# Kernel optimization log

Measured on AMD Instinct MI355X. Metric: run time of the kernel, lower is better.

## Reference

```python
import jax, jax.numpy as jnp
import numpy as np

DIM = 1024
HEADS = 16
DIM_HEAD = DIM // HEADS

def setup_inputs() -> dict:
    key = jax.random.key(0)
    k1, k2, k3 = jax.random.split(key, 3)
    x = jax.random.normal(k1, (2, 2048, DIM), dtype=jnp.float32)
    # nn.Linear(dim, 3*dim, bias=False): weight [3*dim, dim]; y = x @ W.T
    W_qkv = jax.random.normal(k2, (3 * DIM, DIM), dtype=jnp.float32) * (1.0 / np.sqrt(DIM))
    W_out = jax.random.normal(k3, (DIM, DIM), dtype=jnp.float32) * (1.0 / np.sqrt(DIM))
    return {"x": x, "W_qkv": W_qkv, "W_out": W_out}

def reference(x, W_qkv, W_out):
    b, s, _ = x.shape
    scale = DIM_HEAD ** -0.5
    qkv = x @ W_qkv.T                              # [b, s, 3*dim]
    q, k, v = jnp.split(qkv, 3, axis=-1)
    def to_heads(t):
        return t.reshape(b, s, HEADS, DIM_HEAD).transpose(0, 2, 1, 3)  # [b,h,s,d]
    q, k, v = map(to_heads, (q, k, v))
    scores = jnp.einsum('bhid,bhjd->bhij', q, k) * scale
    causal_mask = jnp.triu(jnp.ones((s, s), dtype=bool), k=1)
    scores = jnp.where(causal_mask, -jnp.inf, scores)
    attn = jax.nn.softmax(scores, axis=-1)
    out = jnp.einsum('bhij,bhjd->bhid', attn, v)
    out = out.transpose(0, 2, 1, 3).reshape(b, s, HEADS * DIM_HEAD)
    return out @ W_out.T
```

## Files before the change

### kernel.cpp

```cpp
#include <hip/hip_runtime.h>
#include <hip/hip_bf16.h>
#include <math.h>

using bf16 = __hip_bfloat16;
typedef __attribute__((ext_vector_type(8))) short bf16x8;
typedef __attribute__((ext_vector_type(4))) short bf16x4;
typedef __attribute__((ext_vector_type(4))) float f32x4;
typedef __attribute__((ext_vector_type(2))) int i32x2;

static __device__ __forceinline__ void gl_lds16(const void* g, void* l) {
  __builtin_amdgcn_global_load_lds(
      (const __attribute__((address_space(1))) unsigned int*)g,
      (__attribute__((address_space(3))) unsigned int*)l, 16, 0, 0);
}

#define MFMA16 __builtin_amdgcn_mfma_f32_16x16x32_bf16
#define MFMA16K16 __builtin_amdgcn_mfma_f32_16x16x16bf16_1k

static __device__ __forceinline__ short f2bf(float f) {
  return (short)((__builtin_bit_cast(unsigned int, f) + 0x8000u) >> 16);
}

__global__ __launch_bounds__(256) void cvt_all(
    const float* __restrict__ x, const float* __restrict__ wqkv,
    const float* __restrict__ wout, bf16* __restrict__ xb,
    bf16* __restrict__ wqkvb, bf16* __restrict__ woutb) {
  const int blk = blockIdx.x;
  const float* src;
  bf16* dst;
  int base;
  if (blk < 4096) {
    src = x; dst = xb; base = blk;
  } else if (blk < 7168) {
    src = wqkv; dst = wqkvb; base = blk - 4096;
  } else {
    src = wout; dst = woutb; base = blk - 7168;
  }
  const int i = (base * 256 + threadIdx.x) * 4;
  const float4 v = *(const float4*)(src + i);
  bf16x4 o;
  o.x = f2bf(v.x);
  o.y = f2bf(v.y);
  o.z = f2bf(v.z);
  o.w = f2bf(v.w);
  *(bf16x4*)(dst + i) = o;
}

template <int K>
static __device__ __forceinline__ void gemm_bt_acc(
    const bf16* __restrict__ A, const bf16* __restrict__ B,
    int rowA0, int rowB0, bf16* As, bf16* Bs, f32x4 acc[4][4]) {
  const int t = threadIdx.x;
  const int w = t >> 6, l = t & 63;
  const int quad = l >> 4, l16 = l & 15;
  const int wm = (w >> 1) * 64, wn = (w & 1) * 64;
  const int c0 = t, c1 = t + 256;
  const bf16* a0 = A + (size_t)(rowA0 + (c0 >> 2)) * K + (c0 & 3) * 8;
  const bf16* a1 = A + (size_t)(rowA0 + (c1 >> 2)) * K + (c1 & 3) * 8;
  const bf16* b0 = B + (size_t)(rowB0 + (c0 >> 2)) * K + (c0 & 3) * 8;
  const bf16* b1 = B + (size_t)(rowB0 + (c1 >> 2)) * K + (c1 & 3) * 8;
  for (int k0 = 0; k0 < K; k0 += 32) {
    __syncthreads();
    gl_lds16(a0 + k0, As + c0 * 8);
    gl_lds16(a1 + k0, As + c1 * 8);
    gl_lds16(b0 + k0, Bs + c0 * 8);
    gl_lds16(b1 + k0, Bs + c1 * 8);
    __syncthreads();
    bf16x8 af[4], bg[4];
#pragma unroll
    for (int i = 0; i < 4; i++)
      af[i] = *(const bf16x8*)(As + (wm + i * 16 + l16) * 32 + quad * 8);
#pragma unroll
    for (int j = 0; j < 4; j++)
      bg[j] = *(const bf16x8*)(Bs + (wn + j * 16 + l16) * 32 + quad * 8);
#pragma unroll
    for (int i = 0; i < 4; i++)
#pragma unroll
      for (int j = 0; j < 4; j++)
        acc[i][j] = MFMA16(af[i], bg[j], acc[i][j], 0, 0, 0);
  }
}

__global__ __launch_bounds__(256) void qkv_gemm(
    const bf16* __restrict__ x, const bf16* __restrict__ Wqkv,
    bf16* __restrict__ Qb, bf16* __restrict__ Kb, bf16* __restrict__ Vt) {
  __shared__ bf16 As[128 * 32];
  __shared__ bf16 Bs[128 * 32];
  f32x4 acc[4][4];
#pragma unroll
  for (int i = 0; i < 4; i++)
#pragma unroll
    for (int j = 0; j < 4; j++) acc[i][j] = (f32x4){0.f, 0.f, 0.f, 0.f};
  const int bm = blockIdx.x, bn = blockIdx.y;
  gemm_bt_acc<1024>(x, Wqkv, bm * 128, bn * 128, As, Bs, acc);

  const int t = threadIdx.x, w = t >> 6, l = t & 63;
  const int quad = l >> 4, l16 = l & 15;
  const int wm = (w >> 1) * 64, wn = (w & 1) * 64;
#pragma unroll
  for (int i = 0; i < 4; i++) {
#pragma unroll
    for (int j = 0; j < 4; j++) {
      const int n = bn * 128 + wn + j * 16 + l16;
      const int which = n >> 10;
      const int nn = n & 1023;
      const int h = nn >> 6, d = nn & 63;
      const float sc = (which == 0) ? 0.125f : 1.0f;
#pragma unroll
      for (int r = 0; r < 4; r++) {
        const int m = bm * 128 + wm + i * 16 + quad * 4 + r;
        const int b = m >> 11, s = m & 2047;
        const int bh = b * 16 + h;
        const bf16 v = __float2bfloat16(acc[i][j][r] * sc);
        if (which == 0)
          Qb[((size_t)bh * 2048 + s) * 64 + d] = v;
        else if (which == 1)
          Kb[((size_t)bh * 2048 + s) * 64 + d] = v;
        else
          Vt[((size_t)bh * 64 + d) * 2048 + s] = v;
      }
    }
  }
}

__global__ __launch_bounds__(256) void attn_kernel(
    const bf16* __restrict__ Qb, const bf16* __restrict__ Kb,
    const bf16* __restrict__ Vt, bf16* __restrict__ attn) {
  __shared__ bf16 Qs[64 * 64];
  __shared__ bf16 Ks[128 * 64];
  __shared__ bf16 Vts[64 * 128];
  const int x = blockIdx.x;
  const int bh = x & 31;
  const int idx = x >> 5;
  const int qt = (idx < 16) ? idx : 47 - idx;
  const int q0 = qt * 64;
  const int t = threadIdx.x, w = t >> 6, l = t & 63;
  const int quad = l >> 4, l16 = l & 15;
  const bf16x4 ones = {16256, 16256, 16256, 16256};

  const bf16* Qg = Qb + ((size_t)bh * 2048 + q0) * 64;
#pragma unroll
  for (int c = t; c < 512; c += 256) {
    const int row = c >> 3, pos = c & 7;
    gl_lds16(Qg + (row * 8 + (pos ^ (row & 7))) * 8, Qs + c * 8);
  }

  f32x4 oacc[4];
  f32x4 lacc = (f32x4){0.f, 0.f, 0.f, 0.f};
#pragma unroll
  for (int md = 0; md < 4; md++) oacc[md] = (f32x4){0.f, 0.f, 0.f, 0.f};

  const int njj = (qt + 2) >> 1;
  for (int jj = 0; jj < njj; jj++) {
    const int j0 = jj * 128;
    __syncthreads();
    const bf16* Kg = Kb + ((size_t)bh * 2048 + j0) * 64;
#pragma unroll
    for (int c = t; c < 1024; c += 256) {
      const int row = c >> 3, pos = c & 7;
      gl_lds16(Kg + (row * 8 + (pos ^ (row & 7))) * 8, Ks + c * 8);
    }
    const bf16* Vg = Vt + (size_t)bh * 64 * 2048 + j0;
#pragma unroll
    for (int c = t; c < 1024; c += 256) {
      const int d = c >> 4, pos = c & 15;
      gl_lds16(Vg + (size_t)d * 2048 + ((pos ^ (d & 15)) * 8), Vts + c * 8);
    }
    __syncthreads();

    f32x4 sacc[8];
#pragma unroll
    for (int mt = 0; mt < 8; mt++) sacc[mt] = (f32x4){0.f, 0.f, 0.f, 0.f};
#pragma unroll
    for (int kk = 0; kk < 2; kk++) {
      const int qrow = w * 16 + l16;
      const int qpos = (kk * 4 + quad) ^ (qrow & 7);
      bf16x8 qf = *(const bf16x8*)(Qs + qrow * 64 + qpos * 8);
#pragma unroll
      for (int mt = 0; mt < 8; mt++) {
        const int row = mt * 16 + l16;
        const int pos = (kk * 4 + quad) ^ (row & 7);
        bf16x8 kf = *(const bf16x8*)(Ks + row * 64 + pos * 8);
        sacc[mt] = MFMA16(kf, qf, sacc[mt], 0, 0, 0);
      }
    }

    bf16x4 pfrag[8];
    if (jj == njj - 1) {
      const int qi = q0 + w * 16 + l16;
#pragma unroll
      for (int mt = 0; mt < 8; mt++) {
        unsigned rb[4];
#pragma unroll
        for (int r = 0; r < 4; r++) {
          const int sg = j0 + mt * 16 + quad * 4 + r;
          const float p = (sg <= qi) ? __expf(sacc[mt][r]) : 0.f;
          rb[r] = __builtin_bit_cast(unsigned, p) + 0x8000u;
        }
        i32x2 pk;
        pk.x = (int)__builtin_amdgcn_perm(rb[1], rb[0], 0x07060302u);
        pk.y = (int)__builtin_amdgcn_perm(rb[3], rb[2], 0x07060302u);
        pfrag[mt] = __builtin_bit_cast(bf16x4, pk);
      }
    } else {
#pragma unroll
      for (int mt = 0; mt < 8; mt++) {
        unsigned rb[4];
#pragma unroll
        for (int r = 0; r < 4; r++) {
          const float p = __expf(sacc[mt][r]);
          rb[r] = __builtin_bit_cast(unsigned, p) + 0x8000u;
        }
        i32x2 pk;
        pk.x = (int)__builtin_amdgcn_perm(rb[1], rb[0], 0x07060302u);
        pk.y = (int)__builtin_amdgcn_perm(rb[3], rb[2], 0x07060302u);
        pfrag[mt] = __builtin_bit_cast(bf16x4, pk);
      }
    }

#pragma unroll
    for (int kt = 0; kt < 8; kt++) {
      lacc = MFMA16K16(ones, pfrag[kt], lacc, 0, 0, 0);
#pragma unroll
      for (int md = 0; md < 4; md++) {
        const int d = md * 16 + l16;
        const int pos = (kt * 2 + (quad >> 1)) ^ (d & 15);
        bf16x4 va = *(const bf16x4*)(Vts + d * 128 + pos * 8 + (quad & 1) * 4);
        oacc[md] = MFMA16K16(va, pfrag[kt], oacc[md], 0, 0, 0);
      }
    }
  }

  const float inv = 1.0f / lacc[0];
  const int b = bh >> 4, h = bh & 15;
  const int srow = q0 + w * 16 + l16;
#pragma unroll
  for (int md = 0; md < 4; md++) {
    bf16x4 o4;
#pragma unroll
    for (int r = 0; r < 4; r++) o4[r] = f2bf(oacc[md][r] * inv);
    *(bf16x4*)(attn + ((size_t)b * 2048 + srow) * 1024 + h * 64 + md * 16 +
               quad * 4) = o4;
  }
}

__global__ __launch_bounds__(256) void out_gemm(
    const bf16* __restrict__ attn, const bf16* __restrict__ Wout,
    float* __restrict__ out) {
  __shared__ bf16 As[128 * 32];
  __shared__ bf16 Bs[64 * 32];
  f32x4 acc[4][2];
#pragma unroll
  for (int i = 0; i < 4; i++)
#pragma unroll
    for (int j = 0; j < 2; j++) acc[i][j] = (f32x4){0.f, 0.f, 0.f, 0.f};
  const int bm = blockIdx.x, bn = blockIdx.y;
  const int t = threadIdx.x, w = t >> 6, l = t & 63;
  const int quad = l >> 4, l16 = l & 15;
  const int wm = (w >> 1) * 64, wn = (w & 1) * 32;
  const int c0 = t, c1 = t + 256;
  const bf16* a0 = attn + (size_t)(bm * 128 + (c0 >> 2)) * 1024 + (c0 & 3) * 8;
  const bf16* a1 = attn + (size_t)(bm * 128 + (c1 >> 2)) * 1024 + (c1 & 3) * 8;
  const bf16* b0 = Wout + (size_t)(bn * 64 + (t >> 2)) * 1024 + (t & 3) * 8;
  for (int k0 = 0; k0 < 1024; k0 += 32) {
    __syncthreads();
    gl_lds16(a0 + k0, As + c0 * 8);
    gl_lds16(a1 + k0, As + c1 * 8);
    gl_lds16(b0 + k0, Bs + t * 8);
    __syncthreads();
    bf16x8 af[4], bg[2];
#pragma unroll
    for (int i = 0; i < 4; i++)
      af[i] = *(const bf16x8*)(As + (wm + i * 16 + l16) * 32 + quad * 8);
#pragma unroll
    for (int j = 0; j < 2; j++)
      bg[j] = *(const bf16x8*)(Bs + (wn + j * 16 + l16) * 32 + quad * 8);
#pragma unroll
    for (int i = 0; i < 4; i++)
#pragma unroll
      for (int j = 0; j < 2; j++)
        acc[i][j] = MFMA16(af[i], bg[j], acc[i][j], 0, 0, 0);
  }
#pragma unroll
  for (int i = 0; i < 4; i++) {
#pragma unroll
    for (int j = 0; j < 2; j++) {
      const int n = bn * 64 + wn + j * 16 + l16;
#pragma unroll
      for (int r = 0; r < 4; r++) {
        const int m = bm * 128 + wm + i * 16 + quad * 4 + r;
        out[(size_t)m * 1024 + n] = acc[i][j][r];
      }
    }
  }
}

extern "C" void kernel_launch(void* const* d_in, const int* in_sizes, int n_in,
                              void* d_out, int out_size, void* d_ws, size_t ws_size,
                              hipStream_t stream) {
  const float* x = (const float*)d_in[0];
  const float* Wqkv = (const float*)d_in[1];
  const float* Wout = (const float*)d_in[2];
  float* out = (float*)d_out;

  char* ws = (char*)d_ws;
  const size_t MB = 1024 * 1024;
  bf16* xb = (bf16*)(ws + 0 * MB);
  bf16* at = (bf16*)(ws + 0 * MB);
  bf16* Wqkvb = (bf16*)(ws + 8 * MB);
  bf16* Woutb = (bf16*)(ws + 14 * MB);
  bf16* Qb = (bf16*)(ws + 16 * MB);
  bf16* Kb = (bf16*)(ws + 24 * MB);
  bf16* Vt = (bf16*)(ws + 32 * MB);

  cvt_all<<<8192, 256, 0, stream>>>(x, Wqkv, Wout, xb, Wqkvb, Woutb);
  qkv_gemm<<<dim3(32, 24), 256, 0, stream>>>(xb, Wqkvb, Qb, Kb, Vt);
  attn_kernel<<<1024, 256, 0, stream>>>(Qb, Kb, Vt, at);
  out_gemm<<<dim3(32, 16), 256, 0, stream>>>(at, Woutb, out);
}
```

Before: 169.6 us.

## Pair causal query tiles per attention block and vectorize V-transpose stores

The attention kernel now launches half as many blocks, and each block processes two query tiles (idx and 31-idx), so every block does about the same amount of causal work. This is meant to remove load imbalance and tail effects from blocks with very different KV loop lengths. The price is less parallelism: 512 blocks on the device instead of 1024, each running serially longer. Separately, the QKV GEMM epilogue writes the transposed V output as a 4-wide bf16 vector store instead of four scalar stores, and hoists the batch and sequence index math out of the inner loop.

Result: faster. 166.1 us (-2.0%).

```diff
diff --git a/kernel.cpp b/kernel.cpp
--- a/kernel.cpp
+++ b/kernel.cpp
@@ -99,25 +99,29 @@
   const int wm = (w >> 1) * 64, wn = (w & 1) * 64;
 #pragma unroll
   for (int i = 0; i < 4; i++) {
+    const int m0 = bm * 128 + wm + i * 16 + quad * 4;
+    const int b = m0 >> 11, s0 = m0 & 2047;
 #pragma unroll
     for (int j = 0; j < 4; j++) {
       const int n = bn * 128 + wn + j * 16 + l16;
       const int which = n >> 10;
       const int nn = n & 1023;
       const int h = nn >> 6, d = nn & 63;
-      const float sc = (which == 0) ? 0.125f : 1.0f;
-#pragma unroll
-      for (int r = 0; r < 4; r++) {
-        const int m = bm * 128 + wm + i * 16 + quad * 4 + r;
-        const int b = m >> 11, s = m & 2047;
-        const int bh = b * 16 + h;
-        const bf16 v = __float2bfloat16(acc[i][j][r] * sc);
-        if (which == 0)
-          Qb[((size_t)bh * 2048 + s) * 64 + d] = v;
-        else if (which == 1)
-          Kb[((size_t)bh * 2048 + s) * 64 + d] = v;
-        else
-          Vt[((size_t)bh * 64 + d) * 2048 + s] = v;
+      const int bh = b * 16 + h;
+      if (which == 2) {
+        bf16x4 v4;
+#pragma unroll
+        for (int r = 0; r < 4; r++)
+          v4[r] = (short)__builtin_bit_cast(unsigned short,
+                                            __float2bfloat16(acc[i][j][r]));
+        *(bf16x4*)(Vt + ((size_t)bh * 64 + d) * 2048 + s0) = v4;
+      } else {
+        const float sc = (which == 0) ? 0.125f : 1.0f;
+        bf16* dst = (which == 0) ? Qb : Kb;
+#pragma unroll
+        for (int r = 0; r < 4; r++)
+          dst[((size_t)bh * 2048 + s0 + r) * 64 + d] =
+              __float2bfloat16(acc[i][j][r] * sc);
       }
     }
   }
@@ -132,115 +136,120 @@
   const int x = blockIdx.x;
   const int bh = x & 31;
   const int idx = x >> 5;
-  const int qt = (idx < 16) ? idx : 47 - idx;
-  const int q0 = qt * 64;
   const int t = threadIdx.x, w = t >> 6, l = t & 63;
   const int quad = l >> 4, l16 = l & 15;
   const bf16x4 ones = {16256, 16256, 16256, 16256};
-
-  const bf16* Qg = Qb + ((size_t)bh * 2048 + q0) * 64;
-#pragma unroll
-  for (int c = t; c < 512; c += 256) {
-    const int row = c >> 3, pos = c & 7;
-    gl_lds16(Qg + (row * 8 + (pos ^ (row & 7))) * 8, Qs + c * 8);
-  }
-
-  f32x4 oacc[4];
-  f32x4 lacc = (f32x4){0.f, 0.f, 0.f, 0.f};
-#pragma unroll
-  for (int md = 0; md < 4; md++) oacc[md] = (f32x4){0.f, 0.f, 0.f, 0.f};
-
-  const int njj = (qt + 2) >> 1;
-  for (int jj = 0; jj < njj; jj++) {
-    const int j0 = jj * 128;
-    __syncthreads();
-    const bf16* Kg = Kb + ((size_t)bh * 2048 + j0) * 64;
-#pragma unroll
-    for (int c = t; c < 1024; c += 256) {
+  const int b = bh >> 4, h = bh & 15;
+
+  for (int pass = 0; pass < 2; pass++) {
+    const int qt = pass ? 31 - idx : idx;
+    const int q0 = qt * 64;
+    if (pass) __syncthreads();
+
+    const bf16* Qg = Qb + ((size_t)bh * 2048 + q0) * 64;
+#pragma unroll
+    for (int c = t; c < 512; c += 256) {
       const int row = c >> 3, pos = c & 7;
-      gl_lds16(Kg + (row * 8 + (pos ^ (row & 7))) * 8, Ks + c * 8);
-    }
-    const bf16* Vg = Vt + (size_t)bh * 64 * 2048 + j0;
-#pragma unroll
-    for (int c = t; c < 1024; c += 256) {
-      const int d = c >> 4, pos = c & 15;
-      gl_lds16(Vg + (size_t)d * 2048 + ((pos ^ (d & 15)) * 8), Vts + c * 8);
-    }
-    __syncthreads();
-
-    f32x4 sacc[8];
-#pragma unroll
-    for (int mt = 0; mt < 8; mt++) sacc[mt] = (f32x4){0.f, 0.f, 0.f, 0.f};
-#pragma unroll
-    for (int kk = 0; kk < 2; kk++) {
-      const int qrow = w * 16 + l16;
-      const int qpos = (kk * 4 + quad) ^ (qrow & 7);
-      bf16x8 qf = *(const bf16x8*)(Qs + qrow * 64 + qpos * 8);
-#pragma unroll
-      for (int mt = 0; mt < 8; mt++) {
-        const int row = mt * 16 + l16;
-        const int pos = (kk * 4 + quad) ^ (row & 7);
-        bf16x8 kf = *(const bf16x8*)(Ks + row * 64 + pos * 8);
-        sacc[mt] = MFMA16(kf, qf, sacc[mt], 0, 0, 0);
-      }
-    }
-
-    bf16x4 pfrag[8];
-    if (jj == njj - 1) {
-      const int qi = q0 + w * 16 + l16;
-#pragma unroll
-      for (int mt = 0; mt < 8; mt++) {
-        unsigned rb[4];
-#pragma unroll
-        for (int r = 0; r < 4; r++) {
-          const int sg = j0 + mt * 16 + quad * 4 + r;
-          const float p = (sg <= qi) ? __expf(sacc[mt][r]) : 0.f;
-          rb[r] = __builtin_bit_cast(unsigned, p) + 0x8000u;
+      gl_lds16(Qg + (row * 8 + (pos ^ (row & 7))) * 8, Qs + c * 8);
+    }
+
+    f32x4 oacc[4];
+    f32x4 lacc = (f32x4){0.f, 0.f, 0.f, 0.f};
+#pragma unroll
+    for (int md = 0; md < 4; md++) oacc[md] = (f32x4){0.f, 0.f, 0.f, 0.f};
+
+    const int njj = (qt + 2) >> 1;
+    for (int jj = 0; jj < njj; jj++) {
+      const int j0 = jj * 128;
+      __syncthreads();
+      const bf16* Kg = Kb + ((size_t)bh * 2048 + j0) * 64;
+#pragma unroll
+      for (int c = t; c < 1024; c += 256) {
+        const int row = c >> 3, pos = c & 7;
+        gl_lds16(Kg + (row * 8 + (pos ^ (row & 7))) * 8, Ks + c * 8);
+      }
+      const bf16* Vg = Vt + (size_t)bh * 64 * 2048 + j0;
+#pragma unroll
+      for (int c = t; c < 1024; c += 256) {
+        const int d = c >> 4, pos = c & 15;
+        gl_lds16(Vg + (size_t)d * 2048 + ((pos ^ (d & 15)) * 8), Vts + c * 8);
+      }
+      __syncthreads();
+
+      f32x4 sacc[8];
+#pragma unroll
+      for (int mt = 0; mt < 8; mt++) sacc[mt] = (f32x4){0.f, 0.f, 0.f, 0.f};
+#pragma unroll
+      for (int kk = 0; kk < 2; kk++) {
+        const int qrow = w * 16 + l16;
+        const int qpos = (kk * 4 + quad) ^ (qrow & 7);
+        bf16x8 qf = *(const bf16x8*)(Qs + qrow * 64 + qpos * 8);
+#pragma unroll
+        for (int mt = 0; mt < 8; mt++) {
+          const int row = mt * 16 + l16;
+          const int pos = (kk * 4 + quad) ^ (row & 7);
+          bf16x8 kf = *(const bf16x8*)(Ks + row * 64 + pos * 8);
+          sacc[mt] = MFMA16(kf, qf, sacc[mt], 0, 0, 0);
         }
-        i32x2 pk;
-        pk.x = (int)__builtin_amdgcn_perm(rb[1], rb[0], 0x07060302u);
-        pk.y = (int)__builtin_amdgcn_perm(rb[3], rb[2], 0x07060302u);
-        pfrag[mt] = __builtin_bit_cast(bf16x4, pk);
-      }
-    } else {
-#pragma unroll
-      for (int mt = 0; mt < 8; mt++) {
-        unsigned rb[4];
-#pragma unroll
-        for (int r = 0; r < 4; r++) {
-          const float p = __expf(sacc[mt][r]);
-          rb[r] = __builtin_bit_cast(unsigned, p) + 0x8000u;
+      }
+
+      bf16x4 pfrag[8];
+      if (jj == njj - 1) {
+        const int qi = q0 + w * 16 + l16;
+#pragma unroll
+        for (int mt = 0; mt < 8; mt++) {
+          unsigned rb[4];
+#pragma unroll
+          for (int r = 0; r < 4; r++) {
+            const int sg = j0 + mt * 16 + quad * 4 + r;
+            const float p = (sg <= qi) ? __expf(sacc[mt][r]) : 0.f;
+            rb[r] = __builtin_bit_cast(unsigned, p) + 0x8000u;
+          }
+          i32x2 pk;
+          pk.x = (int)__builtin_amdgcn_perm(rb[1], rb[0], 0x07060302u);
+          pk.y = (int)__builtin_amdgcn_perm(rb[3], rb[2], 0x07060302u);
+          pfrag[mt] = __builtin_bit_cast(bf16x4, pk);
         }
-        i32x2 pk;
-        pk.x = (int)__builtin_amdgcn_perm(rb[1], rb[0], 0x07060302u);
-        pk.y = (int)__builtin_amdgcn_perm(rb[3], rb[2], 0x07060302u);
-        pfrag[mt] = __builtin_bit_cast(bf16x4, pk);
-      }
-    }
-
-#pragma unroll
-    for (int kt = 0; kt < 8; kt++) {
-      lacc = MFMA16K16(ones, pfrag[kt], lacc, 0, 0, 0);
-#pragma unroll
-      for (int md = 0; md < 4; md++) {
-        const int d = md * 16 + l16;
-        const int pos = (kt * 2 + (quad >> 1)) ^ (d & 15);
-        bf16x4 va = *(const bf16x4*)(Vts + d * 128 + pos * 8 + (quad & 1) * 4);
-        oacc[md] = MFMA16K16(va, pfrag[kt], oacc[md], 0, 0, 0);
-      }
-    }
-  }
-
-  const float inv = 1.0f / lacc[0];
-  const int b = bh >> 4, h = bh & 15;
-  const int srow = q0 + w * 16 + l16;
-#pragma unroll
-  for (int md = 0; md < 4; md++) {
-    bf16x4 o4;
-#pragma unroll
-    for (int r = 0; r < 4; r++) o4[r] = f2bf(oacc[md][r] * inv);
-    *(bf16x4*)(attn + ((size_t)b * 2048 + srow) * 1024 + h * 64 + md * 16 +
-               quad * 4) = o4;
+      } else {
+#pragma unroll
+        for (int mt = 0; mt < 8; mt++) {
+          unsigned rb[4];
+#pragma unroll
+          for (int r = 0; r < 4; r++) {
+            const float p = __expf(sacc[mt][r]);
+            rb[r] = __builtin_bit_cast(unsigned, p) + 0x8000u;
+          }
+          i32x2 pk;
+          pk.x = (int)__builtin_amdgcn_perm(rb[1], rb[0], 0x07060302u);
+          pk.y = (int)__builtin_amdgcn_perm(rb[3], rb[2], 0x07060302u);
+          pfrag[mt] = __builtin_bit_cast(bf16x4, pk);
+        }
+      }
+
+#pragma unroll
+      for (int kt = 0; kt < 8; kt++) {
+        lacc = MFMA16K16(ones, pfrag[kt], lacc, 0, 0, 0);
+#pragma unroll
+        for (int md = 0; md < 4; md++) {
+          const int d = md * 16 + l16;
+          const int pos = (kt * 2 + (quad >> 1)) ^ (d & 15);
+          bf16x4 va =
+              *(const bf16x4*)(Vts + d * 128 + pos * 8 + (quad & 1) * 4);
+          oacc[md] = MFMA16K16(va, pfrag[kt], oacc[md], 0, 0, 0);
+        }
+      }
+    }
+
+    const float inv = 1.0f / lacc[0];
+    const int srow = q0 + w * 16 + l16;
+#pragma unroll
+    for (int md = 0; md < 4; md++) {
+      bf16x4 o4;
+#pragma unroll
+      for (int r = 0; r < 4; r++) o4[r] = f2bf(oacc[md][r] * inv);
+      *(bf16x4*)(attn + ((size_t)b * 2048 + srow) * 1024 + h * 64 + md * 16 +
+                 quad * 4) = o4;
+    }
   }
 }
 
@@ -315,6 +324,6 @@
 
   cvt_all<<<8192, 256, 0, stream>>>(x, Wqkv, Wout, xb, Wqkvb, Woutb);
   qkv_gemm<<<dim3(32, 24), 256, 0, stream>>>(xb, Wqkvb, Qb, Kb, Vt);
-  attn_kernel<<<1024, 256, 0, stream>>>(Qb, Kb, Vt, at);
+  attn_kernel<<<512, 256, 0, stream>>>(Qb, Kb, Vt, at);
   out_gemm<<<dim3(32, 16), 256, 0, stream>>>(at, Woutb, out);
 }
```
